# Optimization experiments

Measured on AMD Instinct MI355X. Metric: run time of the kernel, lower is better.

## Reference

```python
import jax, jax.numpy as jnp
import numpy as np

INPUT_DIM, CB_DIM, CB_VOCAB = 512, 16, 8192
N = 16384
EPS = 1e-12  # F.normalize default eps


def setup_inputs() -> dict:
    key = jax.random.key(0)
    kx, kp, kc = jax.random.split(key, 3)
    x = jax.random.normal(kx, (N, INPUT_DIM), dtype=jnp.float32)
    # xavier_uniform_ on P [input_dim, cb_dim]
    bound = float(np.sqrt(6.0 / (INPUT_DIM + CB_DIM)))
    P = jax.random.uniform(kp, (INPUT_DIM, CB_DIM), dtype=jnp.float32,
                           minval=-bound, maxval=bound)
    # CB = F.normalize(randn(cb_vocab, cb_dim)) -> unit rows
    CB = jax.random.normal(kc, (CB_VOCAB, CB_DIM), dtype=jnp.float32)
    CB = CB / jnp.maximum(jnp.linalg.norm(CB, axis=1, keepdims=True), EPS)
    return {"x": x, "P": P, "CB": CB}


def reference(x, P, CB):
    # random projection: [N, input_dim] @ [input_dim, cb_dim] -> [N, cb_dim]
    xp = x @ P
    # L2-normalize projected vectors (rows)
    xp = xp / jnp.maximum(jnp.linalg.norm(xp, axis=1, keepdims=True), EPS)
    # cosine similarity against unit-norm codebook = plain dot product
    sim = xp @ CB.T  # [N, cb_vocab]
    return jnp.argmax(sim, axis=1)  # [N] int codebook indices
```

## Files before the change

kernel.cpp:

```cpp
#include <hip/hip_runtime.h>
#include <stdint.h>

#define N_ROWS   16384
#define IN_DIM   512
#define CB_DIM   16
#define CB_VOCAB 8192

#define PROJ_BLOCKS 512
#define PREP_BLOCKS 128

#define N_RT   (N_ROWS / 16)
#define N_CT   (CB_VOCAB / 16)
#define CODEPARTS 16
#define CT_PER_PART (N_CT / CODEPARTS)
#define N_ROWGRP 64

#define WS_OFF_AFA  0
#define WS_OFF_AFB  (1u << 20)
#define WS_OFF_BHH  (2u << 20)
#define WS_OFF_B31  ((2u << 20) + (512u << 10))
#define WS_OFF_PART (3u << 20)
#define WS_OFF_CNT  ((3u << 20) + (128u << 10))

typedef __attribute__((ext_vector_type(8))) short bf16x8;
typedef __attribute__((ext_vector_type(4))) float f32x4;

__device__ __forceinline__ unsigned fkey(float f) {
    unsigned u = __float_as_uint(f);
    return (u & 0x80000000u) ? ~u : (u | 0x80000000u);
}

__device__ __forceinline__ unsigned short f2bf(float f) {
    unsigned u = __float_as_uint(f);
    return (unsigned short)((u + 0x7FFFu + ((u >> 16) & 1u)) >> 16);
}
__device__ __forceinline__ float bf2f(unsigned short h) {
    return __uint_as_float(((unsigned)h) << 16);
}

__global__ __launch_bounds__(256, 2)
void k_front(const float* __restrict__ x, const float* __restrict__ P,
             const float* __restrict__ CB,
             bf16x8* __restrict__ AfragA, bf16x8* __restrict__ AfragB,
             bf16x8* __restrict__ Bhh, bf16x8* __restrict__ B31,
             unsigned long long* __restrict__ part, unsigned* __restrict__ cnt) {
    __shared__ float4 Ps[IN_DIM * 4];
    __shared__ float  accs[8][32][20];

    const int wave = threadIdx.x >> 6;
    const int lane = threadIdx.x & 63;

    if (blockIdx.x >= PROJ_BLOCKS) {
        const int pb = blockIdx.x - PROJ_BLOCKS;
        if (threadIdx.x < 128) part[pb * 128 + threadIdx.x] = 0ull;
        if (pb == 0 && threadIdx.x < 64) cnt[threadIdx.x] = 0u;

        const int ct   = pb * 4 + wave;
        const int n    = lane & 15;
        const int quad = lane >> 4;
        const int kh   = (quad & 1) * 8;
        const int lvl  = quad >> 1;
        const int code = ct * 16 + n;

        const float4* b4 = (const float4*)(CB + (size_t)code * CB_DIM + kh);
        float4 a = b4[0], b = b4[1];
        float v[8] = {a.x, a.y, a.z, a.w, b.x, b.y, b.z, b.w};

        bf16x8 shh, s31;
#pragma unroll
        for (int j = 0; j < 8; ++j) {
            float f = v[j];
            unsigned short b1 = f2bf(f);  float r1 = f - bf2f(b1);
            unsigned short b2 = f2bf(r1); float r2 = r1 - bf2f(b2);
            unsigned short b3 = f2bf(r2);
            shh[j] = (short)(lvl ? b2 : b1);
            s31[j] = (short)(lvl ? b1 : b3);
        }
        Bhh[(size_t)ct * 64 + lane] = shh;
        B31[(size_t)ct * 64 + lane] = s31;
        return;
    }

    const int b = blockIdx.x;
    for (int i = threadIdx.x; i < IN_DIM * 4; i += 256)
        Ps[i] = ((const float4*)P)[i];
    __syncthreads();

    const int r32   = lane & 31;
    const int khalf = lane >> 5;
    const int row   = b * 32 + r32;
    const int kb    = 128 * wave + 64 * khalf;

    float acc[16];
#pragma unroll
    for (int c = 0; c < 16; ++c) acc[c] = 0.0f;

    const float4* xr = (const float4*)(x + (size_t)row * IN_DIM + kb);

#pragma unroll 4
    for (int i = 0; i < 16; ++i) {
        float4 xv = xr[i];
        float xs[4] = {xv.x, xv.y, xv.z, xv.w};
#pragma unroll
        for (int kk = 0; kk < 4; ++kk) {
#pragma unroll
            for (int q = 0; q < 4; ++q) {
                float4 pv = Ps[(kb + 4 * i + kk) * 4 + q];
                acc[4 * q + 0] += xs[kk] * pv.x;
                acc[4 * q + 1] += xs[kk] * pv.y;
                acc[4 * q + 2] += xs[kk] * pv.z;
                acc[4 * q + 3] += xs[kk] * pv.w;
            }
        }
    }

    const int pslot = wave * 2 + khalf;
#pragma unroll
    for (int c = 0; c < 16; ++c) accs[pslot][r32][c] = acc[c];
    __syncthreads();

    if (threadIdx.x < 128) {
        const int rtl  = threadIdx.x >> 6;
        const int l2   = threadIdx.x & 63;
        const int m    = l2 & 15;
        const int quad = l2 >> 4;
        const int kh   = (quad & 1) * 8;
        const int lvl  = quad >> 1;
        const int rloc = rtl * 16 + m;

        float v[8];
#pragma unroll
        for (int j = 0; j < 8; ++j) v[j] = 0.0f;
#pragma unroll
        for (int p = 0; p < 8; ++p) {
#pragma unroll
            for (int j = 0; j < 8; ++j) v[j] += accs[p][rloc][kh + j];
        }

        bf16x8 sa, sb;
#pragma unroll
        for (int j = 0; j < 8; ++j) {
            float f = v[j];
            unsigned short b1 = f2bf(f);  float r1 = f - bf2f(b1);
            unsigned short b2 = f2bf(r1); float r2 = r1 - bf2f(b2);
            unsigned short b3 = f2bf(r2);
            sa[j] = (short)(lvl ? b2 : b1);
            sb[j] = (short)(lvl ? b3 : b1);
        }
        AfragA[(size_t)(2 * b + rtl) * 64 + l2] = sa;
        AfragB[(size_t)(2 * b + rtl) * 64 + l2] = sb;
    }
}

__global__ __launch_bounds__(256, 4)
void k_scan(const bf16x8* __restrict__ AfragA, const bf16x8* __restrict__ AfragB,
            const bf16x8* __restrict__ Bhh, const bf16x8* __restrict__ B31,
            unsigned long long* __restrict__ part, unsigned* __restrict__ cnt,
            int* __restrict__ out) {
    __shared__ int s_done;
    const int codepart = blockIdx.x & (CODEPARTS - 1);
    const int rowgrp   = blockIdx.x >> 4;
    const int wave     = threadIdx.x >> 6;
    const int lane     = threadIdx.x & 63;
    const int n        = lane & 15;
    const int quad     = lane >> 4;
    const int rt_base  = rowgrp * 16 + wave * 4;

    bf16x8 Aa[4], Ab[4];
#pragma unroll
    for (int t = 0; t < 4; ++t) {
        Aa[t] = AfragA[(size_t)(rt_base + t) * 64 + lane];
        Ab[t] = AfragB[(size_t)(rt_base + t) * 64 + lane];
    }

    float bestv[4][4];
    int   bestc[4][4];
#pragma unroll
    for (int t = 0; t < 4; ++t)
#pragma unroll
        for (int r = 0; r < 4; ++r) { bestv[t][r] = -INFINITY; bestc[t][r] = 0; }

    const int ct0 = codepart * CT_PER_PART;
    size_t ib = (size_t)ct0 * 64;
    bf16x8 nb1  = Bhh[ib + lane];
    bf16x8 nb1s = Bhh[ib + (lane ^ 32)];
    bf16x8 nb3  = B31[ib + lane];

    for (int c = 0; c < CT_PER_PART; ++c) {
        bf16x8 b1 = nb1, b1s = nb1s, b3 = nb3;
        if (c + 1 < CT_PER_PART) {
            size_t ibn = (size_t)(ct0 + c + 1) * 64;
            nb1  = Bhh[ibn + lane];
            nb1s = Bhh[ibn + (lane ^ 32)];
            nb3  = B31[ibn + lane];
        }
#pragma unroll
        for (int t = 0; t < 4; ++t) {
            f32x4 s = __builtin_amdgcn_mfma_f32_16x16x32_bf16(
                          Aa[t], b1, (f32x4){0.f, 0.f, 0.f, 0.f}, 0, 0, 0);
            s = __builtin_amdgcn_mfma_f32_16x16x32_bf16(Aa[t], b1s, s, 0, 0, 0);
            s = __builtin_amdgcn_mfma_f32_16x16x32_bf16(Ab[t], b3,  s, 0, 0, 0);
#pragma unroll
            for (int r = 0; r < 4; ++r) {
                if (s[r] > bestv[t][r]) { bestv[t][r] = s[r]; bestc[t][r] = c; }
            }
        }
    }

#pragma unroll
    for (int t = 0; t < 4; ++t) {
#pragma unroll
        for (int r = 0; r < 4; ++r) {
            unsigned code = (unsigned)(codepart * 512 + bestc[t][r] * 16 + n);
            unsigned long long packed =
                ((unsigned long long)fkey(bestv[t][r]) << 32) |
                (unsigned long long)(0xFFFFFFFFu - code);
#pragma unroll
            for (int mk = 1; mk <= 8; mk <<= 1) {
                unsigned long long o = __shfl_xor(packed, mk, 64);
                packed = (o > packed) ? o : packed;
            }
            if (n == 0) {
                int row = (rt_base + t) * 16 + quad * 4 + r;
                atomicMax(&part[row], packed);
            }
        }
    }

    __syncthreads();
    if (threadIdx.x == 0)
        s_done = (atomicAdd(&cnt[rowgrp], 1u) == (unsigned)(CODEPARTS - 1));
    __syncthreads();

    if (s_done) {
        int row = rowgrp * 256 + threadIdx.x;
        unsigned long long v = atomicAdd(&part[row], 0ull);
        out[row] = (int)(0xFFFFFFFFu - (unsigned)(v & 0xFFFFFFFFull));
    }
}

extern "C" void kernel_launch(void* const* d_in, const int* in_sizes, int n_in,
                              void* d_out, int out_size, void* d_ws, size_t ws_size,
                              hipStream_t stream) {
    const float* x  = (const float*)d_in[0];
    const float* P  = (const float*)d_in[1];
    const float* CB = (const float*)d_in[2];
    int* out = (int*)d_out;

    char* ws = (char*)d_ws;
    bf16x8* AfragA = (bf16x8*)(ws + WS_OFF_AFA);
    bf16x8* AfragB = (bf16x8*)(ws + WS_OFF_AFB);
    bf16x8* Bhh    = (bf16x8*)(ws + WS_OFF_BHH);
    bf16x8* B31    = (bf16x8*)(ws + WS_OFF_B31);
    unsigned long long* part = (unsigned long long*)(ws + WS_OFF_PART);
    unsigned* cnt  = (unsigned*)(ws + WS_OFF_CNT);

    k_front<<<PROJ_BLOCKS + PREP_BLOCKS, 256, 0, stream>>>(
        x, P, CB, AfragA, AfragB, Bhh, B31, part, cnt);
    k_scan<<<N_ROWGRP * CODEPARTS, 256, 0, stream>>>(
        AfragA, AfragB, Bhh, B31, part, cnt, out);
}
```

Measured before the change: 114.4 us.

## Stage codebook tiles through double-buffered LDS shared across waves in scan kernel

Before, each wave loaded every codebook tile straight from global memory (three loads per tile, one of them a lane-swizzled duplicate). Now the block's four waves load groups of eight tiles cooperatively into a double-buffered shared-memory buffer, prefetching the next group during the MFMA work and reading the fragments from LDS. This aims to cut redundant global/L2 traffic by four and turn the swizzled reload into an LDS read. In exchange it adds a block barrier per group, extra LDS traffic and about 32KB of LDS per block, which may limit occupancy.

```diff
diff --git a/kernel.cpp b/kernel.cpp
--- a/kernel.cpp
+++ b/kernel.cpp
@@ -14,6 +14,8 @@
 #define CODEPARTS 16
 #define CT_PER_PART (N_CT / CODEPARTS)
 #define N_ROWGRP 64
+#define GRP    8
+#define NGRP   (CT_PER_PART / GRP)
 
 #define WS_OFF_AFA  0
 #define WS_OFF_AFB  (1u << 20)
@@ -157,6 +159,7 @@
             const bf16x8* __restrict__ Bhh, const bf16x8* __restrict__ B31,
             unsigned long long* __restrict__ part, unsigned* __restrict__ cnt,
             int* __restrict__ out) {
+    __shared__ bf16x8 Bs[2][2][GRP][64];
     __shared__ int s_done;
     const int codepart = blockIdx.x & (CODEPARTS - 1);
     const int rowgrp   = blockIdx.x >> 4;
@@ -181,30 +184,52 @@
         for (int r = 0; r < 4; ++r) { bestv[t][r] = -INFINITY; bestc[t][r] = 0; }
 
     const int ct0 = codepart * CT_PER_PART;
-    size_t ib = (size_t)ct0 * 64;
-    bf16x8 nb1  = Bhh[ib + lane];
-    bf16x8 nb1s = Bhh[ib + (lane ^ 32)];
-    bf16x8 nb3  = B31[ib + lane];
-
-    for (int c = 0; c < CT_PER_PART; ++c) {
-        bf16x8 b1 = nb1, b1s = nb1s, b3 = nb3;
-        if (c + 1 < CT_PER_PART) {
-            size_t ibn = (size_t)(ct0 + c + 1) * 64;
-            nb1  = Bhh[ibn + lane];
-            nb1s = Bhh[ibn + (lane ^ 32)];
-            nb3  = B31[ibn + lane];
-        }
-#pragma unroll
-        for (int t = 0; t < 4; ++t) {
-            f32x4 s = __builtin_amdgcn_mfma_f32_16x16x32_bf16(
-                          Aa[t], b1, (f32x4){0.f, 0.f, 0.f, 0.f}, 0, 0, 0);
-            s = __builtin_amdgcn_mfma_f32_16x16x32_bf16(Aa[t], b1s, s, 0, 0, 0);
-            s = __builtin_amdgcn_mfma_f32_16x16x32_bf16(Ab[t], b3,  s, 0, 0, 0);
-#pragma unroll
-            for (int r = 0; r < 4; ++r) {
-                if (s[r] > bestv[t][r]) { bestv[t][r] = s[r]; bestc[t][r] = c; }
-            }
-        }
+    const int ctl = wave * 2;
+
+    {
+        size_t cb = (size_t)(ct0 + ctl) * 64 + lane;
+        bf16x8 p0 = Bhh[cb], p1 = Bhh[cb + 64];
+        bf16x8 p2 = B31[cb], p3 = B31[cb + 64];
+        Bs[0][0][ctl][lane] = p0;  Bs[0][0][ctl + 1][lane] = p1;
+        Bs[0][1][ctl][lane] = p2;  Bs[0][1][ctl + 1][lane] = p3;
+    }
+    __syncthreads();
+
+    for (int g = 0; g < NGRP; ++g) {
+        const int bi = g & 1;
+
+        bf16x8 st0, st1, st2, st3;
+        if (g + 1 < NGRP) {
+            size_t cb = (size_t)(ct0 + (g + 1) * GRP + ctl) * 64 + lane;
+            st0 = Bhh[cb];  st1 = Bhh[cb + 64];
+            st2 = B31[cb];  st3 = B31[cb + 64];
+        }
+
+#pragma unroll
+        for (int cc = 0; cc < GRP; ++cc) {
+            bf16x8 b1  = Bs[bi][0][cc][lane];
+            bf16x8 b1s = Bs[bi][0][cc][lane ^ 32];
+            bf16x8 b3  = Bs[bi][1][cc][lane];
+            const int c = g * GRP + cc;
+#pragma unroll
+            for (int t = 0; t < 4; ++t) {
+                f32x4 s = __builtin_amdgcn_mfma_f32_16x16x32_bf16(
+                              Aa[t], b1, (f32x4){0.f, 0.f, 0.f, 0.f}, 0, 0, 0);
+                s = __builtin_amdgcn_mfma_f32_16x16x32_bf16(Aa[t], b1s, s, 0, 0, 0);
+                s = __builtin_amdgcn_mfma_f32_16x16x32_bf16(Ab[t], b3,  s, 0, 0, 0);
+#pragma unroll
+                for (int r = 0; r < 4; ++r) {
+                    if (s[r] > bestv[t][r]) { bestv[t][r] = s[r]; bestc[t][r] = c; }
+                }
+            }
+        }
+
+        if (g + 1 < NGRP) {
+            const int nbi = bi ^ 1;
+            Bs[nbi][0][ctl][lane] = st0;  Bs[nbi][0][ctl + 1][lane] = st1;
+            Bs[nbi][1][ctl][lane] = st2;  Bs[nbi][1][ctl + 1][lane] = st3;
+        }
+        __syncthreads();
     }
 
 #pragma unroll
```

After: 130.6 us. 1.14x slower.

## Compute two rows per thread in projection and split codebook scan finer

Applied to the files above, without the earlier changes.

The projection kernel now handles 64 rows per block, with each thread accumulating two rows. This reuses every LDS load of P for twice the FMAs and halves the projection block count, and all four waves now build the bf16 fragments instead of two. The scan kernel splits the codebook into 32 parts instead of 16, doubling the grid, and raises the launch-bounds occupancy hint to 8 blocks. The trade-off is more register pressure in the front kernel, plus more atomics and repeated A-fragment loads in the scan.

```diff
diff --git a/kernel.cpp b/kernel.cpp
--- a/kernel.cpp
+++ b/kernel.cpp
@@ -6,12 +6,12 @@
 #define CB_DIM   16
 #define CB_VOCAB 8192
 
-#define PROJ_BLOCKS 512
+#define PROJ_BLOCKS 256
 #define PREP_BLOCKS 128
 
 #define N_RT   (N_ROWS / 16)
 #define N_CT   (CB_VOCAB / 16)
-#define CODEPARTS 16
+#define CODEPARTS 32
 #define CT_PER_PART (N_CT / CODEPARTS)
 #define N_ROWGRP 64
 
@@ -45,7 +45,7 @@
              bf16x8* __restrict__ Bhh, bf16x8* __restrict__ B31,
              unsigned long long* __restrict__ part, unsigned* __restrict__ cnt) {
     __shared__ float4 Ps[IN_DIM * 4];
-    __shared__ float  accs[8][32][20];
+    __shared__ float  accs[8][64][20];
 
     const int wave = threadIdx.x >> 6;
     const int lane = threadIdx.x & 63;
@@ -88,40 +88,49 @@
 
     const int r32   = lane & 31;
     const int khalf = lane >> 5;
-    const int row   = b * 32 + r32;
+    const int row0  = b * 64 + r32;
     const int kb    = 128 * wave + 64 * khalf;
 
-    float acc[16];
-#pragma unroll
-    for (int c = 0; c < 16; ++c) acc[c] = 0.0f;
-
-    const float4* xr = (const float4*)(x + (size_t)row * IN_DIM + kb);
+    float acc0[16], acc1[16];
+#pragma unroll
+    for (int c = 0; c < 16; ++c) { acc0[c] = 0.0f; acc1[c] = 0.0f; }
+
+    const float4* xr0 = (const float4*)(x + (size_t)row0 * IN_DIM + kb);
+    const float4* xr1 = (const float4*)(x + (size_t)(row0 + 32) * IN_DIM + kb);
 
 #pragma unroll 4
     for (int i = 0; i < 16; ++i) {
-        float4 xv = xr[i];
-        float xs[4] = {xv.x, xv.y, xv.z, xv.w};
+        float4 xv0 = xr0[i], xv1 = xr1[i];
+        float xs0[4] = {xv0.x, xv0.y, xv0.z, xv0.w};
+        float xs1[4] = {xv1.x, xv1.y, xv1.z, xv1.w};
 #pragma unroll
         for (int kk = 0; kk < 4; ++kk) {
 #pragma unroll
             for (int q = 0; q < 4; ++q) {
                 float4 pv = Ps[(kb + 4 * i + kk) * 4 + q];
-                acc[4 * q + 0] += xs[kk] * pv.x;
-                acc[4 * q + 1] += xs[kk] * pv.y;
-                acc[4 * q + 2] += xs[kk] * pv.z;
-                acc[4 * q + 3] += xs[kk] * pv.w;
+                acc0[4 * q + 0] += xs0[kk] * pv.x;
+                acc0[4 * q + 1] += xs0[kk] * pv.y;
+                acc0[4 * q + 2] += xs0[kk] * pv.z;
+                acc0[4 * q + 3] += xs0[kk] * pv.w;
+                acc1[4 * q + 0] += xs1[kk] * pv.x;
+                acc1[4 * q + 1] += xs1[kk] * pv.y;
+                acc1[4 * q + 2] += xs1[kk] * pv.z;
+                acc1[4 * q + 3] += xs1[kk] * pv.w;
             }
         }
     }
 
     const int pslot = wave * 2 + khalf;
 #pragma unroll
-    for (int c = 0; c < 16; ++c) accs[pslot][r32][c] = acc[c];
-    __syncthreads();
-
-    if (threadIdx.x < 128) {
-        const int rtl  = threadIdx.x >> 6;
-        const int l2   = threadIdx.x & 63;
+    for (int c = 0; c < 16; ++c) {
+        accs[pslot][r32][c]      = acc0[c];
+        accs[pslot][r32 + 32][c] = acc1[c];
+    }
+    __syncthreads();
+
+    {
+        const int rtl  = wave;
+        const int l2   = lane;
         const int m    = l2 & 15;
         const int quad = l2 >> 4;
         const int kh   = (quad & 1) * 8;
@@ -147,19 +156,19 @@
             sa[j] = (short)(lvl ? b2 : b1);
             sb[j] = (short)(lvl ? b3 : b1);
         }
-        AfragA[(size_t)(2 * b + rtl) * 64 + l2] = sa;
-        AfragB[(size_t)(2 * b + rtl) * 64 + l2] = sb;
-    }
-}
-
-__global__ __launch_bounds__(256, 4)
+        AfragA[(size_t)(4 * b + rtl) * 64 + l2] = sa;
+        AfragB[(size_t)(4 * b + rtl) * 64 + l2] = sb;
+    }
+}
+
+__global__ __launch_bounds__(256, 8)
 void k_scan(const bf16x8* __restrict__ AfragA, const bf16x8* __restrict__ AfragB,
             const bf16x8* __restrict__ Bhh, const bf16x8* __restrict__ B31,
             unsigned long long* __restrict__ part, unsigned* __restrict__ cnt,
             int* __restrict__ out) {
     __shared__ int s_done;
     const int codepart = blockIdx.x & (CODEPARTS - 1);
-    const int rowgrp   = blockIdx.x >> 4;
+    const int rowgrp   = blockIdx.x >> 5;
     const int wave     = threadIdx.x >> 6;
     const int lane     = threadIdx.x & 63;
     const int n        = lane & 15;
@@ -211,7 +220,8 @@
     for (int t = 0; t < 4; ++t) {
 #pragma unroll
         for (int r = 0; r < 4; ++r) {
-            unsigned code = (unsigned)(codepart * 512 + bestc[t][r] * 16 + n);
+            unsigned code = (unsigned)(codepart * (CT_PER_PART * 16) +
+                                       bestc[t][r] * 16 + n);
             unsigned long long packed =
                 ((unsigned long long)fkey(bestv[t][r]) << 32) |
                 (unsigned long long)(0xFFFFFFFFu - code);
```

Result: slower. 294.8 us (+157.7%).

## Stage x through swizzled double-buffered LDS and split codebook scan finer

Applied to the files above, without the earlier changes.

The projection kernel now loads x rows cooperatively with coalesced float4 reads into a swizzled, double-buffered LDS tile. Each thread prefetches the next chunk while computing on the current one, and the tile reuses the shared buffer that later holds the partial accumulators. Occupancy hint for the front kernel is raised to 3 blocks per CU. The scan kernel doubles the number of code partitions to 32, giving twice as many blocks with shorter loops, at the cost of more atomics and more blocks per row group.

```diff
diff --git a/kernel.cpp b/kernel.cpp
--- a/kernel.cpp
+++ b/kernel.cpp
@@ -11,7 +11,7 @@
 
 #define N_RT   (N_ROWS / 16)
 #define N_CT   (CB_VOCAB / 16)
-#define CODEPARTS 16
+#define CODEPARTS 32
 #define CT_PER_PART (N_CT / CODEPARTS)
 #define N_ROWGRP 64
 
@@ -38,14 +38,14 @@
     return __uint_as_float(((unsigned)h) << 16);
 }
 
-__global__ __launch_bounds__(256, 2)
+__global__ __launch_bounds__(256, 3)
 void k_front(const float* __restrict__ x, const float* __restrict__ P,
              const float* __restrict__ CB,
              bf16x8* __restrict__ AfragA, bf16x8* __restrict__ AfragB,
              bf16x8* __restrict__ Bhh, bf16x8* __restrict__ B31,
              unsigned long long* __restrict__ part, unsigned* __restrict__ cnt) {
     __shared__ float4 Ps[IN_DIM * 4];
-    __shared__ float  accs[8][32][20];
+    __shared__ __align__(16) float uni[8 * 32 * 20];
 
     const int wave = threadIdx.x >> 6;
     const int lane = threadIdx.x & 63;
@@ -81,47 +81,69 @@
         return;
     }
 
-    const int b = blockIdx.x;
-    for (int i = threadIdx.x; i < IN_DIM * 4; i += 256)
+    const int b   = blockIdx.x;
+    const int tid = threadIdx.x;
+
+#define XS(bf, r, c) uni[((bf) * 2176) + (r) * 68 + (c)]
+
+    for (int i = tid; i < IN_DIM * 4; i += 256)
         Ps[i] = ((const float4*)P)[i];
-    __syncthreads();
-
-    const int r32   = lane & 31;
-    const int khalf = lane >> 5;
-    const int row   = b * 32 + r32;
-    const int kb    = 128 * wave + 64 * khalf;
+
+    const int lr   = tid >> 3;
+    const int lc   = tid & 7;
+    const int wcol = (lc ^ ((lr >> 3) & 3)) << 3;
+    const float4* xg = (const float4*)(x + (size_t)(b * 32 + lr) * IN_DIM);
+
+    float4 c0a = xg[lc * 2], c0b = xg[lc * 2 + 1];
+    *(float4*)&XS(0, lr, wcol)     = c0a;
+    *(float4*)&XS(0, lr, wcol + 4) = c0b;
+    float4 n0 = xg[16 + lc * 2], n1 = xg[16 + lc * 2 + 1];
+    __syncthreads();
+
+    const int r32  = tid & 31;
+    const int s    = tid >> 5;
+    const int rcol = (s ^ ((r32 >> 3) & 3)) << 3;
 
     float acc[16];
 #pragma unroll
     for (int c = 0; c < 16; ++c) acc[c] = 0.0f;
 
-    const float4* xr = (const float4*)(x + (size_t)row * IN_DIM + kb);
-
-#pragma unroll 4
-    for (int i = 0; i < 16; ++i) {
-        float4 xv = xr[i];
-        float xs[4] = {xv.x, xv.y, xv.z, xv.w};
-#pragma unroll
-        for (int kk = 0; kk < 4; ++kk) {
+    for (int g = 0; g < 8; ++g) {
+        if (g < 7) {
+            *(float4*)&XS((g + 1) & 1, lr, wcol)     = n0;
+            *(float4*)&XS((g + 1) & 1, lr, wcol + 4) = n1;
+            if (g < 6) {
+                n0 = xg[(g + 2) * 16 + lc * 2];
+                n1 = xg[(g + 2) * 16 + lc * 2 + 1];
+            }
+        }
+
+        float4 xa = *(const float4*)&XS(g & 1, r32, rcol);
+        float4 xb = *(const float4*)&XS(g & 1, r32, rcol + 4);
+        float xv[8] = {xa.x, xa.y, xa.z, xa.w, xb.x, xb.y, xb.z, xb.w};
+        const int kb4 = (g * 64 + s * 8) * 4;
+#pragma unroll
+        for (int j = 0; j < 8; ++j) {
 #pragma unroll
             for (int q = 0; q < 4; ++q) {
-                float4 pv = Ps[(kb + 4 * i + kk) * 4 + q];
-                acc[4 * q + 0] += xs[kk] * pv.x;
-                acc[4 * q + 1] += xs[kk] * pv.y;
-                acc[4 * q + 2] += xs[kk] * pv.z;
-                acc[4 * q + 3] += xs[kk] * pv.w;
-            }
-        }
-    }
-
-    const int pslot = wave * 2 + khalf;
-#pragma unroll
-    for (int c = 0; c < 16; ++c) accs[pslot][r32][c] = acc[c];
-    __syncthreads();
-
-    if (threadIdx.x < 128) {
-        const int rtl  = threadIdx.x >> 6;
-        const int l2   = threadIdx.x & 63;
+                float4 pv = Ps[kb4 + j * 4 + q];
+                acc[4 * q + 0] += xv[j] * pv.x;
+                acc[4 * q + 1] += xv[j] * pv.y;
+                acc[4 * q + 2] += xv[j] * pv.z;
+                acc[4 * q + 3] += xv[j] * pv.w;
+            }
+        }
+        __syncthreads();
+    }
+
+    float (*accs)[32][20] = (float(*)[32][20])uni;
+#pragma unroll
+    for (int c = 0; c < 16; ++c) accs[s][r32][c] = acc[c];
+    __syncthreads();
+
+    if (tid < 128) {
+        const int rtl  = tid >> 6;
+        const int l2   = tid & 63;
         const int m    = l2 & 15;
         const int quad = l2 >> 4;
         const int kh   = (quad & 1) * 8;
@@ -150,6 +172,7 @@
         AfragA[(size_t)(2 * b + rtl) * 64 + l2] = sa;
         AfragB[(size_t)(2 * b + rtl) * 64 + l2] = sb;
     }
+#undef XS
 }
 
 __global__ __launch_bounds__(256, 4)
@@ -159,7 +182,7 @@
             int* __restrict__ out) {
     __shared__ int s_done;
     const int codepart = blockIdx.x & (CODEPARTS - 1);
-    const int rowgrp   = blockIdx.x >> 4;
+    const int rowgrp   = blockIdx.x >> 5;
     const int wave     = threadIdx.x >> 6;
     const int lane     = threadIdx.x & 63;
     const int n        = lane & 15;
@@ -211,7 +234,8 @@
     for (int t = 0; t < 4; ++t) {
 #pragma unroll
         for (int r = 0; r < 4; ++r) {
-            unsigned code = (unsigned)(codepart * 512 + bestc[t][r] * 16 + n);
+            unsigned code = (unsigned)(codepart * (CT_PER_PART * 16) +
+                                       bestc[t][r] * 16 + n);
             unsigned long long packed =
                 ((unsigned long long)fkey(bestv[t][r]) << 32) |
                 (unsigned long long)(0xFFFFFFFFu - code);
```

Measured after the change: 118.6 us. 3.7% more time.
